# Optimization experiments

Measured on AMD Instinct MI355X. Metric: run time of the kernel, lower is better.

## Reference

```python
import jax, jax.numpy as jnp
import numpy as np

MIN_NORM = 1e-15
BALL_EPS = 4e-3  # float32 proj eps used by HGCN PoincareBall
C_IN = 1.0
C_OUT = 1.0
N_NODES = 100000
N_EDGES = 1200000
DIM = 64
RATIO = 0.75


def _artanh(x):
    x = jnp.clip(x, -1.0 + 1e-7, 1.0 - 1e-7)
    return 0.5 * (jnp.log1p(x) - jnp.log1p(-x))


def _norm(x):
    return jnp.clip(jnp.linalg.norm(x, axis=-1, keepdims=True), MIN_NORM, None)


def proj(x, c):
    n = _norm(x)
    maxnorm = (1.0 - BALL_EPS) / jnp.sqrt(c)
    return jnp.where(n > maxnorm, x / n * maxnorm, x)


def expmap0(u, c):
    sc = jnp.sqrt(c)
    n = _norm(u)
    return jnp.tanh(sc * n) * u / (sc * n)


def logmap0(p, c):
    sc = jnp.sqrt(c)
    n = _norm(p)
    return _artanh(sc * n) * p / (sc * n)


def mobius_add(x, y, c):
    x2 = jnp.sum(x * x, -1, keepdims=True)
    y2 = jnp.sum(y * y, -1, keepdims=True)
    xy = jnp.sum(x * y, -1, keepdims=True)
    num = (1.0 + 2.0 * c * xy + c * y2) * x + (1.0 - c * x2) * y
    den = 1.0 + 2.0 * c * xy + c * c * x2 * y2
    return num / jnp.clip(den, MIN_NORM, None)


def mobius_matvec(m, x, c):
    sc = jnp.sqrt(c)
    xn = _norm(x)
    mx = x @ m.T  # [N, out]
    mxn = _norm(mx)
    res = jnp.tanh(mxn / xn * _artanh(sc * xn)) * mx / (mxn * sc)
    zero = jnp.all(mx == 0, axis=-1, keepdims=True)
    return jnp.where(zero, jnp.zeros((), mx.dtype), res)


def setup_inputs() -> dict:
    key = jax.random.key(0)
    k1, k2, k3, k4 = jax.random.split(key, 4)
    # points on the Poincare ball (small tangent vectors exp-mapped)
    x = proj(expmap0(0.01 * jax.random.normal(k1, (N_NODES, DIM), jnp.float32), C_IN), C_IN)
    edge_index = jax.random.randint(k2, (2, N_EDGES), 0, N_NODES, dtype=jnp.int32)
    xav = float(np.sqrt(2.0) * np.sqrt(6.0 / (DIM + DIM)))  # xavier_uniform gain sqrt(2) scale
    weight = jax.random.uniform(k3, (DIM, DIM), jnp.float32, -xav, xav)
    bias = jnp.zeros((DIM,), jnp.float32)
    lw_w = jax.random.normal(k4, (1, 2 * DIM), jnp.float32) * 0.05
    lw_b = jnp.zeros((1,), jnp.float32)
    return {"x": x, "edge_index": edge_index, "weight": weight, "bias": bias, "lw_w": lw_w, "lw_b": lw_b}


def reference(x, edge_index, weight, bias, lw_w, lw_b):
    N = x.shape[0]
    # ---- HypLinear (eval mode, dropout=0) ----
    h = proj(mobius_matvec(weight, x, C_IN), C_IN)
    hyp_bias = proj(expmap0(bias[None, :], C_IN), C_IN)  # proj_tan0 is identity on Poincare ball
    h = proj(mobius_add(h, hyp_bias, C_IN), C_IN)
    # ---- NodeSelect ----
    x_tan = logmap0(h, C_IN)  # [N, D]
    src, dst = edge_index[0], edge_index[1]
    agg = lambda v: jax.ops.segment_sum(v[src], dst, num_segments=N)  # scatter-add over edges
    sum_neigh = agg(x_tan)
    # NodeInformationScore: (I - D^{-1/2} A D^{-1/2}) x with self-loops removed from A
    w = (src != dst).astype(x_tan.dtype)
    deg = jax.ops.segment_sum(w, src, num_segments=N)
    dinv = jnp.where(deg > 0, deg ** -0.5, 0.0)
    norm_w = -(dinv[src] * w * dinv[dst])  # [E]
    info = x_tan + jax.ops.segment_sum(norm_w[:, None] * x_tan[src], dst, num_segments=N)
    score = jnp.sum(jnp.abs(info), axis=1)  # [N]
    k = int(N * RATIO)
    top_vals, _ = jax.lax.top_k(score, k)
    T = top_vals[k - 1]  # min of top-k
    sel = (score > T).astype(x_tan.dtype)[:, None]  # hot_prob mask [N,1]
    sum_sel = agg(sel * x_tan)
    gate = jax.nn.sigmoid(jnp.concatenate([sum_sel, sum_neigh], axis=-1) @ lw_w.T + lw_b)  # [N,1]
    a_x = jax.nn.relu(agg(gate * sel * x_tan))
    out = x_tan + a_x
    out = proj(expmap0(out, C_IN), C_IN)
    # ---- HypAct (relu) ----
    out = jax.nn.relu(out)
    out = proj(expmap0(out, C_OUT), C_OUT)
    return out
```

## Files before the change

### kernel.cpp

```cpp
#include <hip/hip_runtime.h>
#include <hip/hip_fp16.h>
#include <math.h>


#define MAXN_D 0.996
#define MAXN_F 0.996f
#define NPB 64
#define GPT 512
#define NBMAX 512
#define BCAP 6144
#define BINBLK 256
#define SELB 128
#define SBIN 8192
#define CAND_CAP 16384

typedef unsigned long long ull;

__device__ __forceinline__ double wsumd(double v){
#pragma unroll
  for(int o=32;o;o>>=1) v += __shfl_xor(v,o,64);
  return v;
}
__device__ __forceinline__ float wsumf(float v){
#pragma unroll
  for(int o=32;o;o>>=1) v += __shfl_xor(v,o,64);
  return v;
}
__device__ __forceinline__ float qsumf(float v){
#pragma unroll
  for(int o=1;o<16;o<<=1) v += __shfl_xor(v,o,64);
  return v;
}

__global__ __launch_bounds__(256) void k_init(
    const float* __restrict__ bias, double* __restrict__ hb,
    double* __restrict__ hb2, int* __restrict__ rem, int kth,
    int* __restrict__ dstCur, int* __restrict__ srcCur, int NB){
  if(threadIdx.x < 64){
    int lane = threadIdx.x;
    double b = (double)bias[lane];
    double n = fmax(sqrt(wsumd(b*b)), 1e-15);
    double e = tanh(n)*b/n;
    double en = fmax(sqrt(wsumd(e*e)), 1e-15);
    if(en > MAXN_D) e *= MAXN_D/en;
    hb[lane] = e;
    double s2 = wsumd(e*e);
    if(lane==0) *hb2 = s2;
  }
  if(threadIdx.x == 0) *rem = kth;
  for(int b=threadIdx.x; b<NB; b+=256){
    dstCur[b] = b*BCAP;
    srcCur[b] = b*BCAP;
  }
}

__global__ __launch_bounds__(GPT) void k_fat(
    const int* __restrict__ ei, int E, int NB, int chunk,
    int* __restrict__ dstCur, int* __restrict__ srcCur,
    ull* __restrict__ dstbin, int* __restrict__ srcbin, int binBlocks,
    const float* __restrict__ x, const float* __restrict__ W,
    const double* __restrict__ hb, const double* __restrict__ hb2p,
    const float* __restrict__ lww,
    float* __restrict__ xtf, float* __restrict__ xdl, __half* __restrict__ xth,
    float2* __restrict__ pab, int N){
  __shared__ __align__(16) char smem[35328];
  int tid = threadIdx.x;

  if(blockIdx.x < (unsigned)binBlocks){
    int* dh  = (int*)smem;
    int* sh_ = (int*)(smem + 2048);
    int* db  = (int*)(smem + 4096);
    int* sb  = (int*)(smem + 6144);
    for(int t=tid; t<NB; t+=GPT){ dh[t]=0; sh_[t]=0; }
    __syncthreads();
    int start = blockIdx.x*chunk, end = min(E, start+chunk);
    for(int e=start+tid; e<end; e+=GPT){
      int s = ei[e], d = ei[(size_t)E+e];
      atomicAdd(&dh[d>>8],1);
      if(s!=d) atomicAdd(&sh_[s>>8],1);
    }
    __syncthreads();
    for(int t=tid; t<NB; t+=GPT){
      db[t] = dh[t]  ? atomicAdd(&dstCur[t], dh[t])  : 0;
      sb[t] = sh_[t] ? atomicAdd(&srcCur[t], sh_[t]) : 0;
    }
    __syncthreads();
    for(int t=tid; t<NB; t+=GPT){ dh[t]=db[t]; sh_[t]=sb[t]; }
    __syncthreads();
    for(int e=start+tid; e<end; e+=GPT){
      int s = ei[e], d = ei[(size_t)E+e];
      int p = atomicAdd(&dh[d>>8],1);
      dstbin[p] = ((ull)(unsigned)d<<32) | (unsigned)s;
      if(s!=d){ int p2 = atomicAdd(&sh_[s>>8],1); srcbin[p2] = s; }
    }
    return;
  }

  float*  wf   = (float*)smem;
  float*  xf   = (float*)(smem + 16384);
  double (*r123)[3] = (double(*)[3])(smem + 32768);
  double (*abuf)[2] = (double(*)[2])(smem + 34304);
  for(int a=tid; a<4096; a+=GPT){
    int j = (a>>2)&63;
    int k = ((a>>8)<<2) | (a&3);
    wf[a] = W[j*64 + k];
  }
  int i0 = (blockIdx.x - binBlocks)*NPB;
  for(int idx=tid; idx<NPB*64; idx+=GPT){
    int node = i0 + (idx>>6);
    xf[idx] = (node<N) ? x[(size_t)node*64 + (idx&63)] : 0.f;
  }
  __syncthreads();
  int lane = tid & 63;
  int nb = (tid>>6)*8;
  double acc0=0.0, acc1=0.0, acc2=0.0, acc3=0.0;
  double acc4=0.0, acc5=0.0, acc6=0.0, acc7=0.0;
  const float4* wq = (const float4*)wf;
  const float4* xq = (const float4*)xf;
#pragma unroll 2
  for(int k4=0; k4<16; ++k4){
    float4 w4 = wq[k4*64 + lane];
    double w0=(double)w4.x, w1=(double)w4.y, w2d=(double)w4.z, w3=(double)w4.w;
#define MAC(n, accn) { float4 v = xq[(nb+(n))*16 + k4];                       \
    accn = fma(w0,(double)v.x,accn); accn = fma(w1,(double)v.y,accn);         \
    accn = fma(w2d,(double)v.z,accn); accn = fma(w3,(double)v.w,accn); }
    MAC(0,acc0) MAC(1,acc1) MAC(2,acc2) MAC(3,acc3)
    MAC(4,acc4) MAC(5,acc5) MAC(6,acc6) MAC(7,acc7)
#undef MAC
  }
  double hbl = hb[lane];
#define RED4(A0,A1,A2,A3, OFF) {                                              \
    double xd0 = (double)xf[(nb+(OFF)+0)*64+lane];                            \
    double xd1 = (double)xf[(nb+(OFF)+1)*64+lane];                            \
    double xd2 = (double)xf[(nb+(OFF)+2)*64+lane];                            \
    double xd3 = (double)xf[(nb+(OFF)+3)*64+lane];                            \
    double s1_0 = wsumd(xd0*xd0), s2_0 = wsumd((A0)*(A0)), s3_0 = wsumd((A0)*hbl); \
    double s1_1 = wsumd(xd1*xd1), s2_1 = wsumd((A1)*(A1)), s3_1 = wsumd((A1)*hbl); \
    double s1_2 = wsumd(xd2*xd2), s2_2 = wsumd((A2)*(A2)), s3_2 = wsumd((A2)*hbl); \
    double s1_3 = wsumd(xd3*xd3), s2_3 = wsumd((A3)*(A3)), s3_3 = wsumd((A3)*hbl); \
    if(lane==0){                                                              \
      r123[nb+(OFF)+0][0]=s1_0; r123[nb+(OFF)+0][1]=s2_0; r123[nb+(OFF)+0][2]=s3_0; \
      r123[nb+(OFF)+1][0]=s1_1; r123[nb+(OFF)+1][1]=s2_1; r123[nb+(OFF)+1][2]=s3_1; \
      r123[nb+(OFF)+2][0]=s1_2; r123[nb+(OFF)+2][1]=s2_2; r123[nb+(OFF)+2][2]=s3_2; \
      r123[nb+(OFF)+3][0]=s1_3; r123[nb+(OFF)+3][1]=s2_3; r123[nb+(OFF)+3][2]=s3_3; \
    } }
  RED4(acc0,acc1,acc2,acc3, 0)
  RED4(acc4,acc5,acc6,acc7, 4)
#undef RED4
  __syncthreads();
  if(tid < 64){
    double x2s = r123[tid][0], m2 = r123[tid][1], mh = r123[tid][2];
    double y2 = *hb2p;
    double xn  = fmax(sqrt(x2s), 1e-15);
    double mxn = fmax(sqrt(m2), 1e-15);
    double xc  = fmin(fmax(xn, -1.0+1e-7), 1.0-1e-7);
    double at  = 0.5*(log1p(xc)-log1p(-xc));
    double f1  = tanh(mxn/xn*at)/mxn;
    if(m2 == 0.0) f1 = 0.0;
    double h2 = f1*f1*m2;
    double hn = fmax(sqrt(h2), 1e-15);
    if(hn > MAXN_D){ double s = MAXN_D/hn; f1 *= s; h2 = f1*f1*m2; }
    double xy = f1*mh;
    double den = fmax(1.0 + 2.0*xy + h2*y2, 1e-15);
    double a = (1.0 + 2.0*xy + y2)/den;
    double bb = (1.0 - h2)/den;
    double p2 = a*a*h2 + 2.0*a*bb*xy + bb*bb*y2;
    double pn = fmax(sqrt(p2), 1e-15);
    if(pn > MAXN_D){ double s = MAXN_D/pn; a*=s; bb*=s; pn = fmax(pn*s, 1e-15); }
    double nc  = fmin(fmax(pn, -1.0+1e-7), 1.0-1e-7);
    double at2 = 0.5*(log1p(nc)-log1p(-nc));
    double sc  = at2/pn;
    abuf[tid][0] = sc*a*f1;
    abuf[tid][1] = sc*bb;
  }
  __syncthreads();
  float wAl = lww[lane], wBl = lww[64+lane];
#define EMIT(n, accn) { int nd=i0+nb+(n); if(nd<N){                           \
    double al = abuf[nb+(n)][0], be = abuf[nb+(n)][1];                        \
    double v = al*(accn) + be*hbl;                                            \
    float vf = (float)v;                                                      \
    float df = (float)(v - (double)vf);                                       \
    xtf[(size_t)nd*64+lane] = vf;                                             \
    xdl[(size_t)nd*64+lane] = df;                                             \
    xth[(size_t)nd*64+lane] = __float2half(vf);                               \
    float pA = wsumf(vf*wAl);                                                 \
    float pB = wsumf(vf*wBl);                                                 \
    if(lane==0) pab[nd] = make_float2(pA,pB); } }
  EMIT(0,acc0) EMIT(1,acc1) EMIT(2,acc2) EMIT(3,acc3)
  EMIT(4,acc4) EMIT(5,acc5) EMIT(6,acc6) EMIT(7,acc7)
#undef EMIT
}

__global__ __launch_bounds__(256) void k_bucketAB(
    const ull* __restrict__ dstbin, const int* __restrict__ dstCur,
    int* __restrict__ rowbeg, int* __restrict__ rowcnt, int* __restrict__ csr,
    const int* __restrict__ srcbin, const int* __restrict__ srcCur,
    double* __restrict__ dinv, int N){
  int b = blockIdx.x;
  int node0 = b<<8;
  int nodes = min(256, N-node0);
  __shared__ int c[256], ex[256];
  int t = threadIdx.x;
  {
    int base = b*BCAP, cnt = dstCur[b]-base;
    c[t]=0; __syncthreads();
    for(int e=base+t; e<base+cnt; e+=256){
      int d = (int)(dstbin[e]>>32);
      atomicAdd(&c[d-node0],1);
    }
    __syncthreads();
    int v = c[t]; ex[t]=v; __syncthreads();
    for(int off=1; off<256; off<<=1){
      int a = (t>=off) ? ex[t-off] : 0; __syncthreads();
      ex[t] += a; __syncthreads();
    }
    int mybase = base + ex[t] - v;
    if(t<nodes){ rowbeg[node0+t] = mybase; rowcnt[node0+t] = v; }
    c[t] = mybase;
    __syncthreads();
    for(int e=base+t; e<base+cnt; e+=256){
      ull pr = dstbin[e];
      int d = (int)(pr>>32);
      int p = atomicAdd(&c[d-node0],1);
      csr[p] = (int)(pr & 0xffffffffu);
    }
  }
  __syncthreads();
  {
    int base = b*BCAP, cnt = srcCur[b]-base;
    c[t]=0; __syncthreads();
    for(int e=base+t; e<base+cnt; e+=256)
      atomicAdd(&c[srcbin[e]-node0],1);
    __syncthreads();
    if(t<nodes){ int d = c[t]; dinv[node0+t] = (d>0) ? 1.0/sqrt((double)d) : 0.0; }
  }
}

__global__ void k_gatherA(const int* __restrict__ csr, const int* __restrict__ rowbeg,
                          const int* __restrict__ rowcnt,
                          const float* __restrict__ xtf, const float* __restrict__ xdl,
                          const double* __restrict__ dinv,
                          ull* __restrict__ keys, int N){
  int lane = threadIdx.x & 63;
  int i = (int)((blockIdx.x*(unsigned)blockDim.x + threadIdx.x)>>6);
  if(i>=N) return;
  int beg = rowbeg[i], deg = rowcnt[i];
  int g = lane>>3, t = lane&7;
  double di = dinv[i];
  double a0=0,a1=0,a2=0,a3=0,a4=0,a5=0,a6=0,a7=0;
  int j = g;
  int s = (j<deg) ? csr[beg+j] : 0;
  while(j < deg){
    int snext = (j+8<deg) ? csr[beg+j+8] : 0;
    if(s != i){
      double w = di*dinv[s];
      const float4* row = (const float4*)(xtf + (size_t)s*64 + t*8);
      float4 u = row[0], v = row[1];
      a0 -= w*(double)u.x; a1 -= w*(double)u.y; a2 -= w*(double)u.z; a3 -= w*(double)u.w;
      a4 -= w*(double)v.x; a5 -= w*(double)v.y; a6 -= w*(double)v.z; a7 -= w*(double)v.w;
    }
    s = snext; j += 8;
  }
#define XG(v) { v += __shfl_xor(v,8,64); v += __shfl_xor(v,16,64); v += __shfl_xor(v,32,64); }
  XG(a0) XG(a1) XG(a2) XG(a3) XG(a4) XG(a5) XG(a6) XG(a7)
#undef XG
  const float4* xr = (const float4*)(xtf + (size_t)i*64 + t*8);
  const float4* dr = (const float4*)(xdl + (size_t)i*64 + t*8);
  float4 x0 = xr[0], x1 = xr[1], d0 = dr[0], d1 = dr[1];
  double sc =
    fabs(((double)x0.x+(double)d0.x)+a0) + fabs(((double)x0.y+(double)d0.y)+a1) +
    fabs(((double)x0.z+(double)d0.z)+a2) + fabs(((double)x0.w+(double)d0.w)+a3) +
    fabs(((double)x1.x+(double)d1.x)+a4) + fabs(((double)x1.y+(double)d1.y)+a5) +
    fabs(((double)x1.z+(double)d1.z)+a6) + fabs(((double)x1.w+(double)d1.w)+a7);
  sc += __shfl_xor(sc,1,64); sc += __shfl_xor(sc,2,64); sc += __shfl_xor(sc,4,64);
  if(lane==0) keys[i] = (ull)__double_as_longlong(sc);
}

__global__ __launch_bounds__(256) void k_sel13(
    const ull* __restrict__ keys, int N,
    ull* __restrict__ pref, int* __restrict__ rem,
    int lev, int shift, int width,
    int* __restrict__ hist , int* __restrict__ ticket){
  __shared__ int h[SBIN];
  __shared__ int part[256];
  __shared__ int lastflag, pickedD, pickedR;
  int t = threadIdx.x;
  for(int b=t; b<SBIN; b+=256) h[b] = 0;
  __syncthreads();
  ull p0 = *pref;
  int rem0 = *rem;
  int mask = (1<<width) - 1;
  for(int i = blockIdx.x*256 + t; i<N; i += SELB*256){
    ull kk = keys[i];
    if(lev==0 || (kk >> (shift+width)) == (p0 >> (shift+width)))
      atomicAdd(&h[(int)((kk>>shift)&mask)], 1);
  }
  __syncthreads();
  for(int b=t; b<SBIN; b+=256)
    if(h[b]) __hip_atomic_fetch_add(&hist[b], h[b],
                                    __ATOMIC_RELAXED, __HIP_MEMORY_SCOPE_AGENT);
  __threadfence();
  if(t==0){
    int tk = __hip_atomic_fetch_add(ticket, 1, __ATOMIC_ACQ_REL, __HIP_MEMORY_SCOPE_AGENT);
    lastflag = (tk == SELB-1);
  }
  __syncthreads();
  if(!lastflag) return;
  int base = SBIN-1 - 32*t;
  int pt = 0;
  for(int m=0;m<32;m++)
    pt += __hip_atomic_load(&hist[base-m], __ATOMIC_RELAXED, __HIP_MEMORY_SCOPE_AGENT);
  part[t] = pt;
  __syncthreads();
  for(int off=1; off<256; off<<=1){
    int a = (t>=off) ? part[t-off] : 0; __syncthreads();
    part[t] += a; __syncthreads();
  }
  int cumt = part[t];
  int prev = (t==0) ? 0 : part[t-1];
  if(cumt >= rem0 && prev < rem0){
    int c = 0;
    for(int m=0;m<32;m++){
      int hv = __hip_atomic_load(&hist[base-m], __ATOMIC_RELAXED, __HIP_MEMORY_SCOPE_AGENT);
      c += hv;
      if(prev + c >= rem0){ pickedD = base-m; pickedR = rem0 - (prev + c - hv); break; }
    }
  }
  __syncthreads();
  if(t==0){
    *rem = pickedR;
    *pref = p0 | ((ull)pickedD << shift);
  }
}

__global__ __launch_bounds__(256) void k_finish(
    const ull* __restrict__ keys, int N,
    ull* __restrict__ pref, const int* __restrict__ rem,
    ull* __restrict__ cand, int* __restrict__ cnt, int* __restrict__ ticket){
  __shared__ ull sc[4096];
  __shared__ int lastflag;
  __shared__ ull winner;
  int t = threadIdx.x;
  ull p0 = *pref;
  for(int i = blockIdx.x*256 + t; i<N; i += SELB*256){
    ull kk = keys[i];
    if((kk>>38) == (p0>>38)){
      int idx = __hip_atomic_fetch_add(cnt, 1, __ATOMIC_RELAXED, __HIP_MEMORY_SCOPE_AGENT);
      if(idx < CAND_CAP)
        __hip_atomic_store(&cand[idx], kk, __ATOMIC_RELAXED, __HIP_MEMORY_SCOPE_AGENT);
    }
  }
  __threadfence();
  __syncthreads();
  if(t==0){
    int tk = __hip_atomic_fetch_add(ticket, 1, __ATOMIC_ACQ_REL, __HIP_MEMORY_SCOPE_AGENT);
    lastflag = (tk == SELB-1);
  }
  __syncthreads();
  if(!lastflag) return;
  int C = __hip_atomic_load(cnt, __ATOMIC_RELAXED, __HIP_MEMORY_SCOPE_AGENT);
  if(C > 4096) C = 4096;
  for(int j=t; j<C; j+=256)
    sc[j] = __hip_atomic_load(&cand[j], __ATOMIC_RELAXED, __HIP_MEMORY_SCOPE_AGENT);
  __syncthreads();
  int r = *rem;
  for(int j=t; j<C; j+=256){
    ull c = sc[j];
    int gt=0, eq=0;
    for(int m=0;m<C;m++){ ull o = sc[m]; gt += (o>c); eq += (o==c); }
    if(gt <= r-1 && r-1 < gt+eq) winner = c;
  }
  __syncthreads();
  if(t==0) *pref = winner;
}

__global__ void k_qval(const float2* __restrict__ pab, const ull* __restrict__ keys,
                       const ull* __restrict__ pref, float* __restrict__ q, int N){
  int i = blockIdx.x*blockDim.x + threadIdx.x;
  if(i>=N) return;
  float2 p = pab[i];
  q[i] = p.y + ((keys[i] > *pref) ? p.x : 0.f);
}

__global__ void k_gatherC(const int* __restrict__ csr, const int* __restrict__ rowbeg,
                          const int* __restrict__ rowcnt,
                          const float* __restrict__ q,
                          const ull* __restrict__ keys, const ull* __restrict__ pref,
                          const float* __restrict__ lwb,
                          float* __restrict__ gg, int N){
  int lane = threadIdx.x & 63;
  int wid  = (int)((blockIdx.x*(unsigned)blockDim.x + threadIdx.x)>>6);
  int g = lane>>4, t = lane&15;
  int i = wid*4 + g;
  if(i>=N) return;
  int beg = rowbeg[i], end = beg + rowcnt[i];
  float z = 0.f;
  for(int e = beg + t; e < end; e += 16) z += q[csr[e]];
  z = qsumf(z);
  if(t==0){
    float gv = 1.f/(1.f+expf(-(z + lwb[0])));
    gg[i] = (keys[i] > *pref) ? gv : 0.f;
  }
}

__global__ void k_gatherD(const int* __restrict__ csr, const int* __restrict__ rowbeg,
                          const int* __restrict__ rowcnt,
                          const float* __restrict__ xtf, const __half* __restrict__ xth,
                          const float* __restrict__ gg,
                          float* __restrict__ out, int N){
  int lane = threadIdx.x & 63;
  int i = (int)((blockIdx.x*(unsigned)blockDim.x + threadIdx.x)>>6);
  if(i>=N) return;
  int beg = rowbeg[i], deg = rowcnt[i];
  int g = lane>>3, t = lane&7;
  float c0=0,c1=0,c2=0,c3=0,c4=0,c5=0,c6=0,c7=0;
  int j = g;
  int s = (j<deg) ? csr[beg+j] : 0;
  while(j < deg){
    int snext = (j+8<deg) ? csr[beg+j+8] : 0;
    float gv = gg[s];
    if(gv != 0.f){
      float4 raw = *(const float4*)(xth + (size_t)s*64 + t*8);
      const __half2* hp = (const __half2*)&raw;
      float2 p0 = __half22float2(hp[0]);
      float2 p1 = __half22float2(hp[1]);
      float2 p2 = __half22float2(hp[2]);
      float2 p3 = __half22float2(hp[3]);
      c0 = fmaf(gv,p0.x,c0); c1 = fmaf(gv,p0.y,c1); c2 = fmaf(gv,p1.x,c2); c3 = fmaf(gv,p1.y,c3);
      c4 = fmaf(gv,p2.x,c4); c5 = fmaf(gv,p2.y,c5); c6 = fmaf(gv,p3.x,c6); c7 = fmaf(gv,p3.y,c7);
    }
    s = snext; j += 8;
  }
#define XG(v) { v += __shfl_xor(v,8,64); v += __shfl_xor(v,16,64); v += __shfl_xor(v,32,64); }
  XG(c0) XG(c1) XG(c2) XG(c3) XG(c4) XG(c5) XG(c6) XG(c7)
#undef XG
  const float4* xr = (const float4*)(xtf + (size_t)i*64 + t*8);
  float4 x0 = xr[0], x1 = xr[1];
  float v0 = x0.x + fmaxf(c0,0.f), v1 = x0.y + fmaxf(c1,0.f);
  float v2 = x0.z + fmaxf(c2,0.f), v3 = x0.w + fmaxf(c3,0.f);
  float v4 = x1.x + fmaxf(c4,0.f), v5 = x1.y + fmaxf(c5,0.f);
  float v6 = x1.z + fmaxf(c6,0.f), v7 = x1.w + fmaxf(c7,0.f);
  float n2 = v0*v0+v1*v1+v2*v2+v3*v3+v4*v4+v5*v5+v6*v6+v7*v7;
  n2 += __shfl_xor(n2,1,64); n2 += __shfl_xor(n2,2,64); n2 += __shfl_xor(n2,4,64);
  float n = fmaxf(sqrtf(n2), 1e-15f);
  float f = tanhf(n)/n;
  float e0=f*v0,e1=f*v1,e2=f*v2,e3=f*v3,e4=f*v4,e5=f*v5,e6=f*v6,e7=f*v7;
  float en = fmaxf(tanhf(n), 1e-15f);
  if(en > MAXN_F){ float sf = MAXN_F/en;
    e0*=sf;e1*=sf;e2*=sf;e3*=sf;e4*=sf;e5*=sf;e6*=sf;e7*=sf; }
  e0=fmaxf(e0,0.f);e1=fmaxf(e1,0.f);e2=fmaxf(e2,0.f);e3=fmaxf(e3,0.f);
  e4=fmaxf(e4,0.f);e5=fmaxf(e5,0.f);e6=fmaxf(e6,0.f);e7=fmaxf(e7,0.f);
  float m2 = e0*e0+e1*e1+e2*e2+e3*e3+e4*e4+e5*e5+e6*e6+e7*e7;
  m2 += __shfl_xor(m2,1,64); m2 += __shfl_xor(m2,2,64); m2 += __shfl_xor(m2,4,64);
  float nb = fmaxf(sqrtf(m2), 1e-15f);
  float f2 = tanhf(nb)/nb;
  float o0=f2*e0,o1=f2*e1,o2=f2*e2,o3=f2*e3,o4=f2*e4,o5=f2*e5,o6=f2*e6,o7=f2*e7;
  float on = fmaxf(tanhf(nb), 1e-15f);
  if(on > MAXN_F){ float sf = MAXN_F/on;
    o0*=sf;o1*=sf;o2*=sf;o3*=sf;o4*=sf;o5*=sf;o6*=sf;o7*=sf; }
  if(g==0){
    float4* op = (float4*)(out + (size_t)i*64 + t*8);
    op[0] = make_float4(o0,o1,o2,o3);
    op[1] = make_float4(o4,o5,o6,o7);
  }
}

extern "C" void kernel_launch(void* const* d_in, const int* in_sizes, int n_in,
                              void* d_out, int out_size, void* d_ws, size_t ws_size,
                              hipStream_t stream){
  const float* x    = (const float*)d_in[0];
  const int*   ei   = (const int*)d_in[1];
  const float* W    = (const float*)d_in[2];
  const float* bias = (const float*)d_in[3];
  const float* lww  = (const float*)d_in[4];
  const float* lwb  = (const float*)d_in[5];
  int N = in_sizes[0]/64;
  int E = in_sizes[1]/2;
  int kth = (int)((double)N*0.75);
  int NB = (N+255)>>8;
  if(NB > NBMAX) return;
  long long meanPB = (long long)E / (NB > 0 ? NB : 1);
  if(3*meanPB > 2*(long long)BCAP) return;
  int chunk = (E + BINBLK - 1)/BINBLK;
  size_t binEls = (size_t)NB*BCAP + 4096;

  char* ws = (char*)d_ws;
  size_t cur = 0;
  auto alloc = [&](size_t bytes){ size_t o = cur; cur = (cur + bytes + 255) & ~(size_t)255; return o; };
  size_t o_hb   = alloc(64*sizeof(double));
  size_t o_hb2  = alloc(8);
  size_t o_rem  = alloc(4);
  size_t o_zero = cur;
  size_t o_pref = alloc(8);
  size_t o_hist = alloc(2*(size_t)SBIN*4);
  size_t o_tick = alloc(3*4);
  size_t o_cnt  = alloc(4);
  size_t zlen   = cur - o_zero;
  size_t o_cand = alloc((size_t)CAND_CAP*8);
  size_t o_dCur = alloc((size_t)NBMAX*4);
  size_t o_sCur = alloc((size_t)NBMAX*4);
  size_t o_rbeg = alloc((size_t)N*4);
  size_t o_rcnt = alloc((size_t)N*4);
  size_t o_csr  = alloc(binEls*4);
  size_t o_dbin = alloc(binEls*8);
  size_t o_sbin = alloc(binEls*4);
  size_t o_dinv = alloc((size_t)N*8);
  size_t o_keys = alloc((size_t)N*8);
  size_t o_pab  = alloc((size_t)N*8);
  size_t o_q    = alloc((size_t)N*4);
  size_t o_xtf  = alloc((size_t)N*64*4);
  size_t o_xdl  = alloc((size_t)N*64*4);
  size_t o_xth  = alloc((size_t)N*64*2);
  size_t o_gg   = alloc((size_t)N*4);
  if(ws_size < cur) return;

  double* hb     = (double*)(ws+o_hb);
  double* hb2    = (double*)(ws+o_hb2);
  int*    rem    = (int*)(ws+o_rem);
  ull*    pref   = (ull*)(ws+o_pref);
  int*    hist   = (int*)(ws+o_hist);
  int*    tick   = (int*)(ws+o_tick);
  int*    cnt    = (int*)(ws+o_cnt);
  ull*    cand   = (ull*)(ws+o_cand);
  int*    dstCur = (int*)(ws+o_dCur);
  int*    srcCur = (int*)(ws+o_sCur);
  int*    rowbeg = (int*)(ws+o_rbeg);
  int*    rowcnt = (int*)(ws+o_rcnt);
  int*    csr    = (int*)(ws+o_csr);
  ull*    dstbin = (ull*)(ws+o_dbin);
  int*    srcbin = (int*)(ws+o_sbin);
  double* dinv   = (double*)(ws+o_dinv);
  ull*    keys   = (ull*)(ws+o_keys);
  float2* pab    = (float2*)(ws+o_pab);
  float*  q      = (float*)(ws+o_q);
  float*  xtf    = (float*)(ws+o_xtf);
  float*  xdl    = (float*)(ws+o_xdl);
  __half* xth    = (__half*)(ws+o_xth);
  float*  gg     = (float*)(ws+o_gg);

  hipMemsetAsync(ws+o_zero, 0, zlen, stream);

  int nodeBlocks = (N+3)/4;
  int pBlocks    = (N+15)/16;
  int gpBlocks   = (N+NPB-1)/NPB;

  k_init     <<<1, 256, 0, stream>>>(bias, hb, hb2, rem, kth, dstCur, srcCur, NB);
  k_fat      <<<BINBLK + gpBlocks, GPT, 0, stream>>>(
                 ei, E, NB, chunk, dstCur, srcCur, dstbin, srcbin, BINBLK,
                 x, W, hb, hb2, lww, xtf, xdl, xth, pab, N);
  k_bucketAB <<<NB, 256, 0, stream>>>(dstbin, dstCur, rowbeg, rowcnt, csr,
                                      srcbin, srcCur, dinv, N);
  k_gatherA  <<<nodeBlocks, 256, 0, stream>>>(csr, rowbeg, rowcnt, xtf, xdl, dinv, keys, N);
  k_sel13    <<<SELB, 256, 0, stream>>>(keys, N, pref, rem, 0, 51, 13, hist, tick+0);
  k_sel13    <<<SELB, 256, 0, stream>>>(keys, N, pref, rem, 1, 38, 13, hist+SBIN, tick+1);
  k_finish   <<<SELB, 256, 0, stream>>>(keys, N, pref, rem, cand, cnt, tick+2);
  k_qval     <<<(N+255)/256, 256, 0, stream>>>(pab, keys, pref, q, N);
  k_gatherC  <<<pBlocks, 256, 0, stream>>>(csr, rowbeg, rowcnt, q, keys, pref, lwb, gg, N);
  k_gatherD  <<<nodeBlocks, 256, 0, stream>>>(csr, rowbeg, rowcnt, xtf, xth, gg, (float*)d_out, N);
}
```

Baseline: 318.0 us.

## Fold init and bucket kernels into fat kernel with spin-wait dependency

Removes the k_init and k_bucketAB launches. Bias expmap is now computed per block in shared memory, and the cursor init moves into the memset with a base offset added in code. The CSR bucketing blocks are appended to k_fat and spin on a global counter until all binning blocks have finished. This cuts two kernel launches and their inter-kernel gaps. It relies on the binning blocks being scheduled before the waiting bucket blocks to avoid deadlock, which holds in practice because lower block indices dispatch first.

```diff
diff --git a/kernel.cpp b/kernel.cpp
--- a/kernel.cpp
+++ b/kernel.cpp
@@ -32,38 +32,18 @@
   return v;
 }
 
-__global__ __launch_bounds__(256) void k_init(
-    const float* __restrict__ bias, double* __restrict__ hb,
-    double* __restrict__ hb2, int* __restrict__ rem, int kth,
-    int* __restrict__ dstCur, int* __restrict__ srcCur, int NB){
-  if(threadIdx.x < 64){
-    int lane = threadIdx.x;
-    double b = (double)bias[lane];
-    double n = fmax(sqrt(wsumd(b*b)), 1e-15);
-    double e = tanh(n)*b/n;
-    double en = fmax(sqrt(wsumd(e*e)), 1e-15);
-    if(en > MAXN_D) e *= MAXN_D/en;
-    hb[lane] = e;
-    double s2 = wsumd(e*e);
-    if(lane==0) *hb2 = s2;
-  }
-  if(threadIdx.x == 0) *rem = kth;
-  for(int b=threadIdx.x; b<NB; b+=256){
-    dstCur[b] = b*BCAP;
-    srcCur[b] = b*BCAP;
-  }
-}
-
 __global__ __launch_bounds__(GPT) void k_fat(
     const int* __restrict__ ei, int E, int NB, int chunk,
     int* __restrict__ dstCur, int* __restrict__ srcCur,
-    ull* __restrict__ dstbin, int* __restrict__ srcbin, int binBlocks,
+    ull* __restrict__ dstbin, int* __restrict__ srcbin,
+    int binBlocks, int gpBlocks, int* __restrict__ binDone,
+    int* __restrict__ rowbeg, int* __restrict__ rowcnt, int* __restrict__ csr,
+    double* __restrict__ dinv,
     const float* __restrict__ x, const float* __restrict__ W,
-    const double* __restrict__ hb, const double* __restrict__ hb2p,
-    const float* __restrict__ lww,
+    const float* __restrict__ bias, const float* __restrict__ lww,
     float* __restrict__ xtf, float* __restrict__ xdl, __half* __restrict__ xth,
     float2* __restrict__ pab, int N){
-  __shared__ __align__(16) char smem[35328];
+  __shared__ __align__(16) char smem[35904];
   int tid = threadIdx.x;
 
   if(blockIdx.x < (unsigned)binBlocks){
@@ -81,8 +61,8 @@
     }
     __syncthreads();
     for(int t=tid; t<NB; t+=GPT){
-      db[t] = dh[t]  ? atomicAdd(&dstCur[t], dh[t])  : 0;
-      sb[t] = sh_[t] ? atomicAdd(&srcCur[t], sh_[t]) : 0;
+      db[t] = dh[t]  ? t*BCAP + atomicAdd(&dstCur[t], dh[t])  : 0;
+      sb[t] = sh_[t] ? t*BCAP + atomicAdd(&srcCur[t], sh_[t]) : 0;
     }
     __syncthreads();
     for(int t=tid; t<NB; t+=GPT){ dh[t]=db[t]; sh_[t]=sb[t]; }
@@ -93,42 +73,60 @@
       dstbin[p] = ((ull)(unsigned)d<<32) | (unsigned)s;
       if(s!=d){ int p2 = atomicAdd(&sh_[s>>8],1); srcbin[p2] = s; }
     }
+    __threadfence();
+    __syncthreads();
+    if(tid==0)
+      __hip_atomic_fetch_add(binDone, 1, __ATOMIC_RELEASE, __HIP_MEMORY_SCOPE_AGENT);
     return;
   }
 
-  float*  wf   = (float*)smem;
-  float*  xf   = (float*)(smem + 16384);
-  double (*r123)[3] = (double(*)[3])(smem + 32768);
-  double (*abuf)[2] = (double(*)[2])(smem + 34304);
-  for(int a=tid; a<4096; a+=GPT){
-    int j = (a>>2)&63;
-    int k = ((a>>8)<<2) | (a&3);
-    wf[a] = W[j*64 + k];
-  }
-  int i0 = (blockIdx.x - binBlocks)*NPB;
-  for(int idx=tid; idx<NPB*64; idx+=GPT){
-    int node = i0 + (idx>>6);
-    xf[idx] = (node<N) ? x[(size_t)node*64 + (idx&63)] : 0.f;
-  }
-  __syncthreads();
-  int lane = tid & 63;
-  int nb = (tid>>6)*8;
-  double acc0=0.0, acc1=0.0, acc2=0.0, acc3=0.0;
-  double acc4=0.0, acc5=0.0, acc6=0.0, acc7=0.0;
-  const float4* wq = (const float4*)wf;
-  const float4* xq = (const float4*)xf;
+  if(blockIdx.x < (unsigned)(binBlocks + gpBlocks)){
+    float*  wf   = (float*)smem;
+    float*  xf   = (float*)(smem + 16384);
+    double (*r123)[3] = (double(*)[3])(smem + 32768);
+    double (*abuf)[2] = (double(*)[2])(smem + 34304);
+    double* hbL  = (double*)(smem + 35328);
+    double* hb2L = (double*)(smem + 35840);
+    for(int a=tid; a<4096; a+=GPT){
+      int j = (a>>2)&63;
+      int k = ((a>>8)<<2) | (a&3);
+      wf[a] = W[j*64 + k];
+    }
+    int i0 = (blockIdx.x - binBlocks)*NPB;
+    for(int idx=tid; idx<NPB*64; idx+=GPT){
+      int node = i0 + (idx>>6);
+      xf[idx] = (node<N) ? x[(size_t)node*64 + (idx&63)] : 0.f;
+    }
+    __syncthreads();
+    int lane = tid & 63;
+    int nb = (tid>>6)*8;
+    double acc0=0.0, acc1=0.0, acc2=0.0, acc3=0.0;
+    double acc4=0.0, acc5=0.0, acc6=0.0, acc7=0.0;
+    const float4* wq = (const float4*)wf;
+    const float4* xq = (const float4*)xf;
 #pragma unroll 2
-  for(int k4=0; k4<16; ++k4){
-    float4 w4 = wq[k4*64 + lane];
-    double w0=(double)w4.x, w1=(double)w4.y, w2d=(double)w4.z, w3=(double)w4.w;
+    for(int k4=0; k4<16; ++k4){
+      float4 w4 = wq[k4*64 + lane];
+      double w0=(double)w4.x, w1=(double)w4.y, w2d=(double)w4.z, w3=(double)w4.w;
 #define MAC(n, accn) { float4 v = xq[(nb+(n))*16 + k4];                       \
-    accn = fma(w0,(double)v.x,accn); accn = fma(w1,(double)v.y,accn);         \
-    accn = fma(w2d,(double)v.z,accn); accn = fma(w3,(double)v.w,accn); }
-    MAC(0,acc0) MAC(1,acc1) MAC(2,acc2) MAC(3,acc3)
-    MAC(4,acc4) MAC(5,acc5) MAC(6,acc6) MAC(7,acc7)
+      accn = fma(w0,(double)v.x,accn); accn = fma(w1,(double)v.y,accn);       \
+      accn = fma(w2d,(double)v.z,accn); accn = fma(w3,(double)v.w,accn); }
+      MAC(0,acc0) MAC(1,acc1) MAC(2,acc2) MAC(3,acc3)
+      MAC(4,acc4) MAC(5,acc5) MAC(6,acc6) MAC(7,acc7)
 #undef MAC
-  }
-  double hbl = hb[lane];
+    }
+    if(tid < 64){
+      double bb_ = (double)bias[tid];
+      double n = fmax(sqrt(wsumd(bb_*bb_)), 1e-15);
+      double e = tanh(n)*bb_/n;
+      double en = fmax(sqrt(wsumd(e*e)), 1e-15);
+      if(en > MAXN_D) e *= MAXN_D/en;
+      hbL[tid] = e;
+      double s2 = wsumd(e*e);
+      if(tid==0) hb2L[0] = s2;
+    }
+    __syncthreads();
+    double hbl = hbL[lane];
 #define RED4(A0,A1,A2,A3, OFF) {                                              \
     double xd0 = (double)xf[(nb+(OFF)+0)*64+lane];                            \
     double xd1 = (double)xf[(nb+(OFF)+1)*64+lane];                            \
@@ -144,37 +142,37 @@
       r123[nb+(OFF)+2][0]=s1_2; r123[nb+(OFF)+2][1]=s2_2; r123[nb+(OFF)+2][2]=s3_2; \
       r123[nb+(OFF)+3][0]=s1_3; r123[nb+(OFF)+3][1]=s2_3; r123[nb+(OFF)+3][2]=s3_3; \
     } }
-  RED4(acc0,acc1,acc2,acc3, 0)
-  RED4(acc4,acc5,acc6,acc7, 4)
+    RED4(acc0,acc1,acc2,acc3, 0)
+    RED4(acc4,acc5,acc6,acc7, 4)
 #undef RED4
-  __syncthreads();
-  if(tid < 64){
-    double x2s = r123[tid][0], m2 = r123[tid][1], mh = r123[tid][2];
-    double y2 = *hb2p;
-    double xn  = fmax(sqrt(x2s), 1e-15);
-    double mxn = fmax(sqrt(m2), 1e-15);
-    double xc  = fmin(fmax(xn, -1.0+1e-7), 1.0-1e-7);
-    double at  = 0.5*(log1p(xc)-log1p(-xc));
-    double f1  = tanh(mxn/xn*at)/mxn;
-    if(m2 == 0.0) f1 = 0.0;
-    double h2 = f1*f1*m2;
-    double hn = fmax(sqrt(h2), 1e-15);
-    if(hn > MAXN_D){ double s = MAXN_D/hn; f1 *= s; h2 = f1*f1*m2; }
-    double xy = f1*mh;
-    double den = fmax(1.0 + 2.0*xy + h2*y2, 1e-15);
-    double a = (1.0 + 2.0*xy + y2)/den;
-    double bb = (1.0 - h2)/den;
-    double p2 = a*a*h2 + 2.0*a*bb*xy + bb*bb*y2;
-    double pn = fmax(sqrt(p2), 1e-15);
-    if(pn > MAXN_D){ double s = MAXN_D/pn; a*=s; bb*=s; pn = fmax(pn*s, 1e-15); }
-    double nc  = fmin(fmax(pn, -1.0+1e-7), 1.0-1e-7);
-    double at2 = 0.5*(log1p(nc)-log1p(-nc));
-    double sc  = at2/pn;
-    abuf[tid][0] = sc*a*f1;
-    abuf[tid][1] = sc*bb;
-  }
-  __syncthreads();
-  float wAl = lww[lane], wBl = lww[64+lane];
+    __syncthreads();
+    if(tid < 64){
+      double x2s = r123[tid][0], m2 = r123[tid][1], mh = r123[tid][2];
+      double y2 = hb2L[0];
+      double xn  = fmax(sqrt(x2s), 1e-15);
+      double mxn = fmax(sqrt(m2), 1e-15);
+      double xc  = fmin(fmax(xn, -1.0+1e-7), 1.0-1e-7);
+      double at  = 0.5*(log1p(xc)-log1p(-xc));
+      double f1  = tanh(mxn/xn*at)/mxn;
+      if(m2 == 0.0) f1 = 0.0;
+      double h2 = f1*f1*m2;
+      double hn = fmax(sqrt(h2), 1e-15);
+      if(hn > MAXN_D){ double s = MAXN_D/hn; f1 *= s; h2 = f1*f1*m2; }
+      double xy = f1*mh;
+      double den = fmax(1.0 + 2.0*xy + h2*y2, 1e-15);
+      double a = (1.0 + 2.0*xy + y2)/den;
+      double bb = (1.0 - h2)/den;
+      double p2 = a*a*h2 + 2.0*a*bb*xy + bb*bb*y2;
+      double pn = fmax(sqrt(p2), 1e-15);
+      if(pn > MAXN_D){ double s = MAXN_D/pn; a*=s; bb*=s; pn = fmax(pn*s, 1e-15); }
+      double nc  = fmin(fmax(pn, -1.0+1e-7), 1.0-1e-7);
+      double at2 = 0.5*(log1p(nc)-log1p(-nc));
+      double sc  = at2/pn;
+      abuf[tid][0] = sc*a*f1;
+      abuf[tid][1] = sc*bb;
+    }
+    __syncthreads();
+    float wAl = lww[lane], wBl = lww[64+lane];
 #define EMIT(n, accn) { int nd=i0+nb+(n); if(nd<N){                           \
     double al = abuf[nb+(n)][0], be = abuf[nb+(n)][1];                        \
     double v = al*(accn) + be*hbl;                                            \
@@ -186,53 +184,65 @@
     float pA = wsumf(vf*wAl);                                                 \
     float pB = wsumf(vf*wBl);                                                 \
     if(lane==0) pab[nd] = make_float2(pA,pB); } }
-  EMIT(0,acc0) EMIT(1,acc1) EMIT(2,acc2) EMIT(3,acc3)
-  EMIT(4,acc4) EMIT(5,acc5) EMIT(6,acc6) EMIT(7,acc7)
+    EMIT(0,acc0) EMIT(1,acc1) EMIT(2,acc2) EMIT(3,acc3)
+    EMIT(4,acc4) EMIT(5,acc5) EMIT(6,acc6) EMIT(7,acc7)
 #undef EMIT
-}
-
-__global__ __launch_bounds__(256) void k_bucketAB(
-    const ull* __restrict__ dstbin, const int* __restrict__ dstCur,
-    int* __restrict__ rowbeg, int* __restrict__ rowcnt, int* __restrict__ csr,
-    const int* __restrict__ srcbin, const int* __restrict__ srcCur,
-    double* __restrict__ dinv, int N){
-  int b = blockIdx.x;
-  int node0 = b<<8;
-  int nodes = min(256, N-node0);
-  __shared__ int c[256], ex[256];
-  int t = threadIdx.x;
+    return;
+  }
+
   {
-    int base = b*BCAP, cnt = dstCur[b]-base;
-    c[t]=0; __syncthreads();
-    for(int e=base+t; e<base+cnt; e+=256){
-      int d = (int)(dstbin[e]>>32);
-      atomicAdd(&c[d-node0],1);
-    }
-    __syncthreads();
-    int v = c[t]; ex[t]=v; __syncthreads();
-    for(int off=1; off<256; off<<=1){
-      int a = (t>=off) ? ex[t-off] : 0; __syncthreads();
-      ex[t] += a; __syncthreads();
-    }
-    int mybase = base + ex[t] - v;
-    if(t<nodes){ rowbeg[node0+t] = mybase; rowcnt[node0+t] = v; }
-    c[t] = mybase;
-    __syncthreads();
-    for(int e=base+t; e<base+cnt; e+=256){
-      ull pr = dstbin[e];
-      int d = (int)(pr>>32);
-      int p = atomicAdd(&c[d-node0],1);
-      csr[p] = (int)(pr & 0xffffffffu);
-    }
-  }
-  __syncthreads();
-  {
-    int base = b*BCAP, cnt = srcCur[b]-base;
-    c[t]=0; __syncthreads();
-    for(int e=base+t; e<base+cnt; e+=256)
-      atomicAdd(&c[srcbin[e]-node0],1);
-    __syncthreads();
-    if(t<nodes){ int d = c[t]; dinv[node0+t] = (d>0) ? 1.0/sqrt((double)d) : 0.0; }
+    int b = blockIdx.x - binBlocks - gpBlocks;
+    int* c  = (int*)smem;
+    int* ex = (int*)(smem + 1024);
+    if(tid==0){
+      while(__hip_atomic_load(binDone, __ATOMIC_ACQUIRE, __HIP_MEMORY_SCOPE_AGENT)
+            < binBlocks)
+        __builtin_amdgcn_s_sleep(8);
+    }
+    __syncthreads();
+    int node0 = b<<8;
+    int nodes = min(256, N-node0);
+    {
+      int base = b*BCAP, cnt = dstCur[b];
+      if(tid<256) c[tid]=0;
+      __syncthreads();
+      for(int e=base+tid; e<base+cnt; e+=GPT){
+        int d = (int)(dstbin[e]>>32);
+        atomicAdd(&c[d-node0],1);
+      }
+      __syncthreads();
+      int v = (tid<256)? c[tid] : 0;
+      if(tid<256) ex[tid]=v;
+      __syncthreads();
+      for(int off=1; off<256; off<<=1){
+        int a = (tid<256 && tid>=(unsigned)off) ? ex[tid-off] : 0;
+        __syncthreads();
+        if(tid<256) ex[tid]+=a;
+        __syncthreads();
+      }
+      if(tid<256){
+        int mybase = base + ex[tid] - v;
+        if(tid<nodes){ rowbeg[node0+tid] = mybase; rowcnt[node0+tid] = v; }
+        c[tid] = mybase;
+      }
+      __syncthreads();
+      for(int e=base+tid; e<base+cnt; e+=GPT){
+        ull pr = dstbin[e];
+        int d = (int)(pr>>32);
+        int p = atomicAdd(&c[d-node0],1);
+        csr[p] = (int)(pr & 0xffffffffu);
+      }
+    }
+    __syncthreads();
+    {
+      int base = b*BCAP, cnt = srcCur[b];
+      if(tid<256) c[tid]=0;
+      __syncthreads();
+      for(int e=base+tid; e<base+cnt; e+=GPT)
+        atomicAdd(&c[srcbin[e]-node0],1);
+      __syncthreads();
+      if(tid<nodes){ int d = c[tid]; dinv[node0+tid] = (d>0) ? 1.0/sqrt((double)d) : 0.0; }
+    }
   }
 }
 
@@ -278,7 +288,7 @@
 
 __global__ __launch_bounds__(256) void k_sel13(
     const ull* __restrict__ keys, int N,
-    ull* __restrict__ pref, int* __restrict__ rem,
+    ull* __restrict__ pref, int* __restrict__ rem, int kth,
     int lev, int shift, int width,
     int* __restrict__ hist , int* __restrict__ ticket){
   __shared__ int h[SBIN];
@@ -288,7 +298,7 @@
   for(int b=t; b<SBIN; b+=256) h[b] = 0;
   __syncthreads();
   ull p0 = *pref;
-  int rem0 = *rem;
+  int rem0 = (lev==0) ? kth : *rem;
   int mask = (1<<width) - 1;
   for(int i = blockIdx.x*256 + t; i<N; i += SELB*256){
     ull kk = keys[i];
@@ -487,18 +497,17 @@
   char* ws = (char*)d_ws;
   size_t cur = 0;
   auto alloc = [&](size_t bytes){ size_t o = cur; cur = (cur + bytes + 255) & ~(size_t)255; return o; };
-  size_t o_hb   = alloc(64*sizeof(double));
-  size_t o_hb2  = alloc(8);
-  size_t o_rem  = alloc(4);
   size_t o_zero = cur;
   size_t o_pref = alloc(8);
+  size_t o_rem  = alloc(4);
   size_t o_hist = alloc(2*(size_t)SBIN*4);
   size_t o_tick = alloc(3*4);
   size_t o_cnt  = alloc(4);
+  size_t o_done = alloc(4);
+  size_t o_dCur = alloc((size_t)NBMAX*4);
+  size_t o_sCur = alloc((size_t)NBMAX*4);
   size_t zlen   = cur - o_zero;
   size_t o_cand = alloc((size_t)CAND_CAP*8);
-  size_t o_dCur = alloc((size_t)NBMAX*4);
-  size_t o_sCur = alloc((size_t)NBMAX*4);
   size_t o_rbeg = alloc((size_t)N*4);
   size_t o_rcnt = alloc((size_t)N*4);
   size_t o_csr  = alloc(binEls*4);
@@ -514,16 +523,15 @@
   size_t o_gg   = alloc((size_t)N*4);
   if(ws_size < cur) return;
 
-  double* hb     = (double*)(ws+o_hb);
-  double* hb2    = (double*)(ws+o_hb2);
+  ull*    pref   = (ull*)(ws+o_pref);
   int*    rem    = (int*)(ws+o_rem);
-  ull*    pref   = (ull*)(ws+o_pref);
   int*    hist   = (int*)(ws+o_hist);
   int*    tick   = (int*)(ws+o_tick);
   int*    cnt    = (int*)(ws+o_cnt);
-  ull*    cand   = (ull*)(ws+o_cand);
+  int*    binDone= (int*)(ws+o_done);
   int*    dstCur = (int*)(ws+o_dCur);
   int*    srcCur = (int*)(ws+o_sCur);
+  ull*    cand   = (ull*)(ws+o_cand);
   int*    rowbeg = (int*)(ws+o_rbeg);
   int*    rowcnt = (int*)(ws+o_rcnt);
   int*    csr    = (int*)(ws+o_csr);
@@ -544,17 +552,15 @@
   int pBlocks    = (N+15)/16;
   int gpBlocks   = (N+NPB-1)/NPB;
 
-  k_init     <<<1, 256, 0, stream>>>(bias, hb, hb2, rem, kth, dstCur, srcCur, NB);
-  k_fat      <<<BINBLK + gpBlocks, GPT, 0, stream>>>(
-                 ei, E, NB, chunk, dstCur, srcCur, dstbin, srcbin, BINBLK,
-                 x, W, hb, hb2, lww, xtf, xdl, xth, pab, N);
-  k_bucketAB <<<NB, 256, 0, stream>>>(dstbin, dstCur, rowbeg, rowcnt, csr,
-                                      srcbin, srcCur, dinv, N);
-  k_gatherA  <<<nodeBlocks, 256, 0, stream>>>(csr, rowbeg, rowcnt, xtf, xdl, dinv, keys, N);
-  k_sel13    <<<SELB, 256, 0, stream>>>(keys, N, pref, rem, 0, 51, 13, hist, tick+0);
-  k_sel13    <<<SELB, 256, 0, stream>>>(keys, N, pref, rem, 1, 38, 13, hist+SBIN, tick+1);
-  k_finish   <<<SELB, 256, 0, stream>>>(keys, N, pref, rem, cand, cnt, tick+2);
-  k_qval     <<<(N+255)/256, 256, 0, stream>>>(pab, keys, pref, q, N);
-  k_gatherC  <<<pBlocks, 256, 0, stream>>>(csr, rowbeg, rowcnt, q, keys, pref, lwb, gg, N);
-  k_gatherD  <<<nodeBlocks, 256, 0, stream>>>(csr, rowbeg, rowcnt, xtf, xth, gg, (float*)d_out, N);
-}
+  k_fat     <<<BINBLK + gpBlocks + NB, GPT, 0, stream>>>(
+                ei, E, NB, chunk, dstCur, srcCur, dstbin, srcbin,
+                BINBLK, gpBlocks, binDone, rowbeg, rowcnt, csr, dinv,
+                x, W, bias, lww, xtf, xdl, xth, pab, N);
+  k_gatherA <<<nodeBlocks, 256, 0, stream>>>(csr, rowbeg, rowcnt, xtf, xdl, dinv, keys, N);
+  k_sel13   <<<SELB, 256, 0, stream>>>(keys, N, pref, rem, kth, 0, 51, 13, hist, tick+0);
+  k_sel13   <<<SELB, 256, 0, stream>>>(keys, N, pref, rem, kth, 1, 38, 13, hist+SBIN, tick+1);
+  k_finish  <<<SELB, 256, 0, stream>>>(keys, N, pref, rem, cand, cnt, tick+2);
+  k_qval    <<<(N+255)/256, 256, 0, stream>>>(pab, keys, pref, q, N);
+  k_gatherC <<<pBlocks, 256, 0, stream>>>(csr, rowbeg, rowcnt, q, keys, pref, lwb, gg, N);
+  k_gatherD <<<nodeBlocks, 256, 0, stream>>>(csr, rowbeg, rowcnt, xtf, xth, gg, (float*)d_out, N);
+}
```

Result: slower. 388.4 us (+22.1%).
